# Performance work log

Measured on AMD Instinct MI355X. Metric: run time of the kernel, lower is better.

## Reference

```python
import jax, jax.numpy as jnp
from jax import lax
import numpy as np

D_MODEL = 2048
NUM_EXPERTS = 16
NUM_TOKENS = 8192  # must be divisible by NUM_EXPERTS (balanced assignment)


def setup_inputs() -> dict:
    key = jax.random.key(0)
    k1, k2 = jax.random.split(key)
    features = jax.random.normal(k1, (NUM_TOKENS, D_MODEL), dtype=jnp.float32)
    # gate weight (orthogonal init in torch; gaussian is fine for a numerical baseline)
    W = jax.random.normal(k2, (NUM_EXPERTS, D_MODEL), dtype=jnp.float32) * 0.1
    b = jnp.zeros((NUM_EXPERTS,), dtype=jnp.float32)
    return {"features": features, "W": W, "b": b, "is_training": 1}


def _balanced_assignment(scores):
    """Greedy balanced assignment: each expert receives exactly T//E tokens.
    Deterministic stand-in for the cpp auction-based balanced_assignment: scan
    over tokens, each token takes its best-scoring expert with remaining capacity.
    Returns sort_by_expert: token indices sorted (stably) by assigned expert."""
    T, E = scores.shape
    cap_per_expert = T // E

    def step(cap, s):  # cap: [E] remaining capacity, s: [E] token's scores
        masked = jnp.where(cap > 0, s, -jnp.inf)
        e = jnp.argmax(masked)
        return cap.at[e].add(-1), e

    _, tok2exp = lax.scan(step, jnp.full((E,), cap_per_expert, dtype=jnp.int32), scores)
    sort_by_expert = jnp.argsort(tok2exp, stable=True)  # [T] token ids grouped by expert
    return sort_by_expert


def reference(features, W, b, is_training):
    # gating computed under no_grad in the original
    affinities = lax.stop_gradient(features @ W.T + b)  # [T, E]
    T, E = affinities.shape
    cap = T // E

    sort_by_expert = _balanced_assignment(affinities)

    routing_probs = jax.nn.softmax(affinities, axis=1)  # [T, E]

    # gather_scores: permute probs into expert order, pick each token's score for
    # its assigned expert, then un-permute back to original token order.
    sorted_probs = routing_probs[sort_by_expert]                 # [T, E]
    expert_idx = (jnp.arange(T) // cap)[:, None]                 # [T, 1], balanced splits
    gathered = jnp.take_along_axis(sorted_probs, expert_idx, axis=1)  # [T, 1]
    i_sort = jnp.argsort(sort_by_expert)                         # inverse permutation
    gathered_scores = gathered[i_sort]                           # [T, 1]

    return sort_by_expert, gathered_scores
```

## Files before the change

### kernel.cpp

```cpp
#include <hip/hip_runtime.h>
#include <hip/hip_bf16.h>
#include <math.h>

#define T_TOK 8192
#define D_MODEL 2048
#define N_EXP 16
#define CAP 512
#define NSEG (T_TOK / 64)


__device__ __forceinline__ unsigned int f2ord(float f) {
    unsigned int b = __float_as_uint(f);
    return (b & 0x80000000u) ? ~b : (b | 0x80000000u);
}

__global__ __launch_bounds__(512, 4) void gemm_aff_kernel(
    const float* __restrict__ feat, const float* __restrict__ W,
    float* __restrict__ aff)
{
    __shared__ float flds[8][D_MODEL];

    const int tid  = threadIdx.x;
    const int wave = tid >> 6, lane = tid & 63;
    const int tbase = blockIdx.x * 8;

    {
        const float4* src = (const float4*)(feat + (size_t)tbase * D_MODEL);
        float4* dst = (float4*)&flds[0][0];
        #pragma unroll
        for (int i = 0; i < 8; ++i)
            dst[tid + i * 512] = src[tid + i * 512];
    }

    const float* w0 = W + (size_t)(wave * 2) * D_MODEL + lane * 4;
    const float* w1 = w0 + D_MODEL;

    float acc[16];
    #pragma unroll
    for (int i = 0; i < 16; ++i) acc[i] = 0.f;

    float4 wv0 = *(const float4*)(w0);
    float4 wv1 = *(const float4*)(w1);
    __syncthreads();

    #pragma unroll
    for (int j = 0; j < 8; ++j) {
        float4 wn0, wn1;
        if (j < 7) {
            wn0 = *(const float4*)(w0 + (j + 1) * 256);
            wn1 = *(const float4*)(w1 + (j + 1) * 256);
        } else {
            wn0 = wv0; wn1 = wv1;
        }
        const float* fl = &flds[0][0] + j * 256 + lane * 4;
        #pragma unroll
        for (int r = 0; r < 8; ++r) {
            float4 f = *(const float4*)(fl + r * D_MODEL);
            acc[r * 2 + 0] += f.x * wv0.x;
            acc[r * 2 + 0] += f.y * wv0.y;
            acc[r * 2 + 0] += f.z * wv0.z;
            acc[r * 2 + 0] += f.w * wv0.w;
            acc[r * 2 + 1] += f.x * wv1.x;
            acc[r * 2 + 1] += f.y * wv1.y;
            acc[r * 2 + 1] += f.z * wv1.z;
            acc[r * 2 + 1] += f.w * wv1.w;
        }
        wv0 = wn0; wv1 = wn1;
    }

    #pragma unroll
    for (int step = 0; step < 4; ++step) {
        const int m    = 1 << step;
        const int half = 8 >> step;
        const bool hi  = (lane & m) != 0;
        #pragma unroll
        for (int jj = 0; jj < half; ++jj) {
            float send = hi ? acc[jj] : acc[jj + half];
            float recv = __shfl_xor(send, m, 64);
            acc[jj] = (hi ? acc[jj + half] : acc[jj]) + recv;
        }
    }
    acc[0] += __shfl_xor(acc[0], 16, 64);
    acc[0] += __shfl_xor(acc[0], 32, 64);

    if (lane < 16) {
        const int slot = ((lane & 1) << 3) | (((lane >> 1) & 1) << 2)
                       | (((lane >> 2) & 1) << 1) | ((lane >> 3) & 1);
        const int r = slot >> 1, el = slot & 1;
        aff[(size_t)(tbase + r) * N_EXP + wave * 2 + el] = acc[0];
    }
}

__global__ __launch_bounds__(256) void finalize_kernel(
    const float* __restrict__ aff_in, const float* __restrict__ bias,
    unsigned long long* __restrict__ pref, float* __restrict__ probs)
{
    const int t = blockIdx.x * 256 + threadIdx.x;

    float aff[N_EXP];
    const float4* p = (const float4*)(aff_in + (size_t)t * N_EXP);
    #pragma unroll
    for (int q = 0; q < 4; ++q) {
        float4 v = p[q];
        aff[q*4+0] = v.x; aff[q*4+1] = v.y; aff[q*4+2] = v.z; aff[q*4+3] = v.w;
    }
    #pragma unroll
    for (int e = 0; e < N_EXP; ++e) aff[e] += bias[e];

    float m = aff[0];
    #pragma unroll
    for (int e = 1; e < N_EXP; ++e) m = fmaxf(m, aff[e]);
    float s = 0.f;
    #pragma unroll
    for (int e = 0; e < N_EXP; ++e) s += __expf(aff[e] - m);

    float4* pr = (float4*)(probs + (size_t)t * N_EXP);
    #pragma unroll
    for (int q = 0; q < 4; ++q) {
        float4 v;
        v.x = __expf(aff[q*4+0] - m) / s;
        v.y = __expf(aff[q*4+1] - m) / s;
        v.z = __expf(aff[q*4+2] - m) / s;
        v.w = __expf(aff[q*4+3] - m) / s;
        pr[q] = v;
    }

    unsigned long long key[N_EXP];
    #pragma unroll
    for (int j = 0; j < N_EXP; ++j)
        key[j] = ((unsigned long long)f2ord(aff[j]) << 4) | (unsigned long long)(15 - j);
    unsigned long long pk = 0ull;
    unsigned int used = 0;
    for (int r = 0; r < N_EXP; ++r) {
        unsigned long long bk = 0ull; int be = 0;
        for (int j = 0; j < N_EXP; ++j)
            if (!((used >> j) & 1u) && key[j] > bk) { bk = key[j]; be = j; }
        used |= (1u << be);
        pk = (pk << 4) | (unsigned long long)be;
    }
    pref[t] = pk;
}

__global__ __launch_bounds__(512) void events_kernel(
    const unsigned long long* __restrict__ pref, int* __restrict__ evt)
{
    __shared__ unsigned long long prefL[T_TOK];
    __shared__ unsigned long long segmask[N_EXP][NSEG + 1];
    __shared__ int pseg[N_EXP][NSEG + 1];
    __shared__ int rem_cap[N_EXP], fparr[N_EXP];
    __shared__ int s_avail, s_pmin, s_fe, s_seglo;
    __shared__ int evp[N_EXP], evf[N_EXP];

    const int tid  = threadIdx.x;
    const int wave = tid >> 6, lane = tid & 63;
    const unsigned long long lt_mask = (1ull << lane) - 1ull;

    for (int i = tid; i < T_TOK; i += 512) prefL[i] = pref[i];
    if (tid < N_EXP) rem_cap[tid] = CAP;
    if (tid == 0) { s_avail = 0xFFFF; s_seglo = 0; }
    __syncthreads();

    for (int s = wave; s < NSEG; s += 8) {
        int c = (int)(prefL[s * 64 + lane] >> 60);
        #pragma unroll
        for (int e = 0; e < N_EXP; ++e) {
            unsigned long long mm = __ballot(c == e);
            if (lane == e) segmask[e][s] = mm;
        }
    }
    __syncthreads();

    for (int round = 0; round < N_EXP; ++round) {
        const unsigned int avail = (unsigned int)s_avail;

        #pragma unroll
        for (int ee = 0; ee < 2; ++ee) {
            const int e = wave + ee * 8;
            const unsigned long long m0 = segmask[e][lane];
            const unsigned long long m1 = segmask[e][64 + lane];
            const int c0 = (int)__popcll(m0), c1 = (int)__popcll(m1);
            int v0 = c0;
            #pragma unroll
            for (int d = 1; d < 64; d <<= 1) {
                int o = __shfl_up(v0, d, 64);
                if (lane >= d) v0 += o;
            }
            const int excl0 = v0 - c0;
            const int tot0  = __shfl(v0, 63, 64);
            int v1 = c1;
            #pragma unroll
            for (int d = 1; d < 64; d <<= 1) {
                int o = __shfl_up(v1, d, 64);
                if (lane >= d) v1 += o;
            }
            const int excl1 = tot0 + v1 - c1;
            pseg[e][lane]      = excl0;
            pseg[e][64 + lane] = excl1;

            int fp = 0x7FFFFFFF;
            if ((avail >> e) & 1u) {
                const int need = rem_cap[e];
                int segc = -1, kk = 0;
                if (excl0 < need && excl0 + c0 >= need)      { segc = lane;      kk = need - excl0; }
                else if (excl1 < need && excl1 + c1 >= need) { segc = 64 + lane; kk = need - excl1; }
                unsigned long long b = __ballot(segc >= 0);
                if (b) {
                    int l2    = __builtin_ctzll(b);
                    int sstar = __shfl(segc, l2, 64);
                    int k2    = __shfl(kk,   l2, 64);
                    unsigned long long m = segmask[e][sstar];
                    int rr = (int)__popcll(m & lt_mask);
                    bool hit = ((m >> lane) & 1ull) && (rr == k2 - 1);
                    unsigned long long hb = __ballot(hit);
                    fp = sstar * 64 + __builtin_ctzll(hb);
                }
            }
            if (lane == 0) fparr[e] = fp;
        }
        __syncthreads();

        if (tid == 0) {
            int pm = 0x7FFFFFFF, f = 0;
            #pragma unroll
            for (int e = 0; e < N_EXP; ++e)
                if (fparr[e] < pm) { pm = fparr[e]; f = e; }
            s_pmin = pm; s_fe = f;
        }
        __syncthreads();
        const int pmin = s_pmin, fe = s_fe;
        const int segF = pmin >> 6;
        const int seglo = s_seglo;

        if (tid < N_EXP) {
            const int e = tid;
            unsigned long long mlep = ((pmin & 63) == 63) ? ~0ull
                                      : ((1ull << ((pmin & 63) + 1)) - 1ull);
            unsigned long long m = segmask[e][segF];
            rem_cap[e] -= pseg[e][segF] + (int)__popcll(m & mlep);
            segmask[e][segF] = m & ~mlep;
        }
        for (int i = tid; i < (segF - seglo) * N_EXP; i += 512)
            segmask[i & 15][seglo + (i >> 4)] = 0ull;
        if (tid == 0) {
            evp[round] = pmin; evf[round] = fe;
            s_avail = (int)(avail & ~(1u << fe));
            s_seglo = segF;
        }
        __syncthreads();

        if (round < N_EXP - 1) {
            const unsigned int navail = avail & ~(1u << fe);
            for (int s = segF + wave; s < NSEG; s += 8) {
                unsigned long long m = segmask[fe][s];
                if (m) {
                    if ((m >> lane) & 1ull) {
                        unsigned long long pp = prefL[s * 64 + lane];
                        int e2 = (int)(pp >> 60);
                        while (!((navail >> e2) & 1u)) { pp <<= 4; e2 = (int)(pp >> 60); }
                        atomicOr(&segmask[e2][s], 1ull << lane);
                    }
                    if (lane == 0) segmask[fe][s] = 0ull;
                }
            }
        }
        __syncthreads();
    }

    if (tid < N_EXP) { evt[tid] = evp[tid]; evt[N_EXP + tid] = evf[tid]; }
}

__global__ __launch_bounds__(256) void choice_kernel(
    const unsigned long long* __restrict__ pref, const int* __restrict__ evt,
    unsigned char* __restrict__ t2e, int* __restrict__ bcnt)
{
    __shared__ int evp[N_EXP], evf[N_EXP];
    __shared__ int sc[4][N_EXP];
    const int tid = threadIdx.x, b = blockIdx.x;
    const int wave = tid >> 6, lane = tid & 63;
    if (tid < N_EXP) evp[tid] = evt[tid];
    else if (tid < 2 * N_EXP) evf[tid - N_EXP] = evt[tid];
    __syncthreads();

    const int t = b * 256 + tid;
    unsigned int mask = 0xFFFFu;
    #pragma unroll
    for (int j = 0; j < N_EXP; ++j)
        if (evp[j] < t) mask &= ~(1u << evf[j]);

    unsigned long long pp = pref[t];
    int e = (int)(pp >> 60);
    while (!((mask >> e) & 1u)) { pp <<= 4; e = (int)(pp >> 60); }
    t2e[t] = (unsigned char)e;

    #pragma unroll
    for (int e2 = 0; e2 < N_EXP; ++e2) {
        unsigned long long mm = __ballot(e == e2);
        if (lane == e2) sc[wave][e2] = (int)__popcll(mm);
    }
    __syncthreads();
    if (tid < N_EXP)
        bcnt[b * N_EXP + tid] = sc[0][tid] + sc[1][tid] + sc[2][tid] + sc[3][tid];
}

__global__ __launch_bounds__(256) void writeout_kernel(
    const unsigned char* __restrict__ t2e, const int* __restrict__ bcnt,
    const float* __restrict__ probs,
    float* __restrict__ out0, float* __restrict__ out1)
{
    __shared__ int base[N_EXP];
    __shared__ int sc[4][N_EXP];
    const int tid = threadIdx.x, b = blockIdx.x;
    const int wave = tid >> 6, lane = tid & 63;
    const unsigned long long lt_mask = (1ull << lane) - 1ull;

    const int t = b * 256 + tid;
    const int c = (int)t2e[t];

    unsigned long long own = 0ull;
    #pragma unroll
    for (int e2 = 0; e2 < N_EXP; ++e2) {
        unsigned long long mm = __ballot(c == e2);
        if (c == e2) own = mm;
        if (lane == e2) sc[wave][e2] = (int)__popcll(mm);
    }
    if (tid < N_EXP) {
        int s = 0;
        for (int b2 = 0; b2 < b; ++b2) s += bcnt[b2 * N_EXP + tid];
        base[tid] = s;
    }
    __syncthreads();

    int rank = (int)__popcll(own & lt_mask);
    for (int w2 = 0; w2 < wave; ++w2) rank += sc[w2][c];
    const int pos = base[c] + rank;
    out0[c * CAP + pos] = (float)t;
    out1[t] = probs[(size_t)t * N_EXP + c];
}

extern "C" void kernel_launch(void* const* d_in, const int* in_sizes, int n_in,
                              void* d_out, int out_size, void* d_ws, size_t ws_size,
                              hipStream_t stream) {
    const float* feat = (const float*)d_in[0];
    const float* W    = (const float*)d_in[1];
    const float* bias = (const float*)d_in[2];

    float* out = (float*)d_out;
    char*  ws  = (char*)d_ws;

    float* aff               = (float*)ws;
    unsigned long long* pref = (unsigned long long*)(ws + 524288);
    float* probs             = (float*)(ws + 589824);
    int* evt                 = (int*)(ws + 1114112);
    unsigned char* t2e       = (unsigned char*)(ws + 1114240);
    int* bcnt                = (int*)(ws + 1122432);

    hipLaunchKernelGGL(gemm_aff_kernel, dim3(T_TOK / 8), dim3(512), 0, stream,
                       feat, W, aff);
    hipLaunchKernelGGL(finalize_kernel, dim3(T_TOK / 256), dim3(256), 0, stream,
                       aff, bias, pref, probs);
    hipLaunchKernelGGL(events_kernel, dim3(1), dim3(512), 0, stream,
                       pref, evt);
    hipLaunchKernelGGL(choice_kernel, dim3(T_TOK / 256), dim3(256), 0, stream,
                       pref, evt, t2e, bcnt);
    hipLaunchKernelGGL(writeout_kernel, dim3(T_TOK / 256), dim3(256), 0, stream,
                       t2e, bcnt, probs, out, out + T_TOK);
}
```

Baseline: 187.7 us.

## Keep events-kernel state in registers and cut per-round barriers

```diff
diff --git a/kernel.cpp b/kernel.cpp
--- a/kernel.cpp
+++ b/kernel.cpp
@@ -141,27 +141,24 @@
     pref[t] = pk;
 }
 
-__global__ __launch_bounds__(512) void events_kernel(
+__global__ __launch_bounds__(512, 1) void events_kernel(
     const unsigned long long* __restrict__ pref, int* __restrict__ evt)
 {
-    __shared__ unsigned long long prefL[T_TOK];
-    __shared__ unsigned long long segmask[N_EXP][NSEG + 1];
-    __shared__ int pseg[N_EXP][NSEG + 1];
-    __shared__ int rem_cap[N_EXP], fparr[N_EXP];
-    __shared__ int s_avail, s_pmin, s_fe, s_seglo;
-    __shared__ int evp[N_EXP], evf[N_EXP];
+    __shared__ unsigned long long segmask[N_EXP][NSEG];
+    __shared__ int fparr[N_EXP];
 
     const int tid  = threadIdx.x;
     const int wave = tid >> 6, lane = tid & 63;
     const unsigned long long lt_mask = (1ull << lane) - 1ull;
 
-    for (int i = tid; i < T_TOK; i += 512) prefL[i] = pref[i];
-    if (tid < N_EXP) rem_cap[tid] = CAP;
-    if (tid == 0) { s_avail = 0xFFFF; s_seglo = 0; }
-    __syncthreads();
-
-    for (int s = wave; s < NSEG; s += 8) {
-        int c = (int)(prefL[s * 64 + lane] >> 60);
+    unsigned long long myPref[16];
+    #pragma unroll
+    for (int k = 0; k < 16; ++k) myPref[k] = pref[tid + 512 * k];
+
+    #pragma unroll
+    for (int k = 0; k < 16; ++k) {
+        const int s = k * 8 + wave;
+        const int c = (int)(myPref[k] >> 60);
         #pragma unroll
         for (int e = 0; e < N_EXP; ++e) {
             unsigned long long mm = __ballot(c == e);
@@ -170,103 +167,128 @@
     }
     __syncthreads();
 
+    const int eA = wave, eB = wave + 8;
+    int capA = CAP, capB = CAP;
+    unsigned long long m0A = 0, m1A = 0, m0B = 0, m1B = 0;
+    int excl0A = 0, excl1A = 0, excl0B = 0, excl1B = 0;
+    int segF = 0;
+    unsigned long long mlep = 0;
+    unsigned int avail = 0xFFFFu;
+    int myp = 0, myf = 0;
+
     for (int round = 0; round < N_EXP; ++round) {
-        const unsigned int avail = (unsigned int)s_avail;
-
-        #pragma unroll
-        for (int ee = 0; ee < 2; ++ee) {
-            const int e = wave + ee * 8;
-            const unsigned long long m0 = segmask[e][lane];
-            const unsigned long long m1 = segmask[e][64 + lane];
-            const int c0 = (int)__popcll(m0), c1 = (int)__popcll(m1);
-            int v0 = c0;
+        {
+            int exf = (segF < 64) ? __shfl(excl0A, segF, 64) : __shfl(excl1A, segF - 64, 64);
+            unsigned long long mf = (segF < 64) ? __shfl(m0A, segF, 64) : __shfl(m1A, segF - 64, 64);
+            capA -= exf + (int)__popcll(mf & mlep);
+            exf = (segF < 64) ? __shfl(excl0B, segF, 64) : __shfl(excl1B, segF - 64, 64);
+            mf  = (segF < 64) ? __shfl(m0B, segF, 64) : __shfl(m1B, segF - 64, 64);
+            capB -= exf + (int)__popcll(mf & mlep);
+        }
+
+        unsigned long long a0 = segmask[eA][lane];
+        unsigned long long a1 = segmask[eA][64 + lane];
+        unsigned long long b0 = segmask[eB][lane];
+        unsigned long long b1 = segmask[eB][64 + lane];
+        if (lane < segF)            { a0 = 0; b0 = 0; }
+        else if (lane == segF)      { a0 &= ~mlep; b0 &= ~mlep; }
+        if (64 + lane < segF)       { a1 = 0; b1 = 0; }
+        else if (64 + lane == segF) { a1 &= ~mlep; b1 &= ~mlep; }
+        m0A = a0; m1A = a1; m0B = b0; m1B = b1;
+
+        const int c0A = (int)__popcll(a0), c1A = (int)__popcll(a1);
+        const int c0B = (int)__popcll(b0), c1B = (int)__popcll(b1);
+        int v0A = c0A, v1A = c1A, v0B = c0B, v1B = c1B;
+        #pragma unroll
+        for (int d = 1; d < 64; d <<= 1) {
+            int t0 = __shfl_up(v0A, d, 64);
+            int t1 = __shfl_up(v1A, d, 64);
+            int t2 = __shfl_up(v0B, d, 64);
+            int t3 = __shfl_up(v1B, d, 64);
+            if (lane >= d) { v0A += t0; v1A += t1; v0B += t2; v1B += t3; }
+        }
+        const int tot0A = __shfl(v0A, 63, 64);
+        const int tot0B = __shfl(v0B, 63, 64);
+        excl0A = v0A - c0A;
+        excl1A = tot0A + v1A - c1A;
+        excl0B = v0B - c0B;
+        excl1B = tot0B + v1B - c1B;
+
+        int fpA = 0x7FFFFFFF;
+        if ((avail >> eA) & 1u) {
+            const int need = capA;
+            int segc = -1, kk = 0;
+            if (excl0A < need && excl0A + c0A >= need)      { segc = lane;      kk = need - excl0A; }
+            else if (excl1A < need && excl1A + c1A >= need) { segc = 64 + lane; kk = need - excl1A; }
+            unsigned long long bb = __ballot(segc >= 0);
+            if (bb) {
+                int l2    = __builtin_ctzll(bb);
+                int sstar = __shfl(segc, l2, 64);
+                int k2    = __shfl(kk,   l2, 64);
+                unsigned long long msel = (sstar < 64) ? __shfl(a0, sstar, 64)
+                                                       : __shfl(a1, sstar - 64, 64);
+                int rr = (int)__popcll(msel & lt_mask);
+                bool hit = ((msel >> lane) & 1ull) && (rr == k2 - 1);
+                unsigned long long hb = __ballot(hit);
+                fpA = sstar * 64 + __builtin_ctzll(hb);
+            }
+        }
+        int fpB = 0x7FFFFFFF;
+        if ((avail >> eB) & 1u) {
+            const int need = capB;
+            int segc = -1, kk = 0;
+            if (excl0B < need && excl0B + c0B >= need)      { segc = lane;      kk = need - excl0B; }
+            else if (excl1B < need && excl1B + c1B >= need) { segc = 64 + lane; kk = need - excl1B; }
+            unsigned long long bb = __ballot(segc >= 0);
+            if (bb) {
+                int l2    = __builtin_ctzll(bb);
+                int sstar = __shfl(segc, l2, 64);
+                int k2    = __shfl(kk,   l2, 64);
+                unsigned long long msel = (sstar < 64) ? __shfl(b0, sstar, 64)
+                                                       : __shfl(b1, sstar - 64, 64);
+                int rr = (int)__popcll(msel & lt_mask);
+                bool hit = ((msel >> lane) & 1ull) && (rr == k2 - 1);
+                unsigned long long hb = __ballot(hit);
+                fpB = sstar * 64 + __builtin_ctzll(hb);
+            }
+        }
+        if (lane == 0) { fparr[eA] = fpA; fparr[eB] = fpB; }
+        __syncthreads();
+
+        int pmin = 0x7FFFFFFF, fe = 0;
+        #pragma unroll
+        for (int e = 0; e < N_EXP; ++e) {
+            int f = fparr[e];
+            if (f < pmin) { pmin = f; fe = e; }
+        }
+        if (tid == round) { myp = pmin; myf = fe; }
+
+        const int nsegF = pmin >> 6;
+        const unsigned long long nmlep = ((pmin & 63) == 63) ? ~0ull
+                                         : ((1ull << ((pmin & 63) + 1)) - 1ull);
+        const unsigned int navail = avail & ~(1u << fe);
+
+        if (round < N_EXP - 1) {
             #pragma unroll
-            for (int d = 1; d < 64; d <<= 1) {
-                int o = __shfl_up(v0, d, 64);
-                if (lane >= d) v0 += o;
-            }
-            const int excl0 = v0 - c0;
-            const int tot0  = __shfl(v0, 63, 64);
-            int v1 = c1;
-            #pragma unroll
-            for (int d = 1; d < 64; d <<= 1) {
-                int o = __shfl_up(v1, d, 64);
-                if (lane >= d) v1 += o;
-            }
-            const int excl1 = tot0 + v1 - c1;
-            pseg[e][lane]      = excl0;
-            pseg[e][64 + lane] = excl1;
-
-            int fp = 0x7FFFFFFF;
-            if ((avail >> e) & 1u) {
-                const int need = rem_cap[e];
-                int segc = -1, kk = 0;
-                if (excl0 < need && excl0 + c0 >= need)      { segc = lane;      kk = need - excl0; }
-                else if (excl1 < need && excl1 + c1 >= need) { segc = 64 + lane; kk = need - excl1; }
-                unsigned long long b = __ballot(segc >= 0);
-                if (b) {
-                    int l2    = __builtin_ctzll(b);
-                    int sstar = __shfl(segc, l2, 64);
-                    int k2    = __shfl(kk,   l2, 64);
-                    unsigned long long m = segmask[e][sstar];
-                    int rr = (int)__popcll(m & lt_mask);
-                    bool hit = ((m >> lane) & 1ull) && (rr == k2 - 1);
-                    unsigned long long hb = __ballot(hit);
-                    fp = sstar * 64 + __builtin_ctzll(hb);
-                }
-            }
-            if (lane == 0) fparr[e] = fp;
-        }
-        __syncthreads();
-
-        if (tid == 0) {
-            int pm = 0x7FFFFFFF, f = 0;
-            #pragma unroll
-            for (int e = 0; e < N_EXP; ++e)
-                if (fparr[e] < pm) { pm = fparr[e]; f = e; }
-            s_pmin = pm; s_fe = f;
-        }
-        __syncthreads();
-        const int pmin = s_pmin, fe = s_fe;
-        const int segF = pmin >> 6;
-        const int seglo = s_seglo;
-
-        if (tid < N_EXP) {
-            const int e = tid;
-            unsigned long long mlep = ((pmin & 63) == 63) ? ~0ull
-                                      : ((1ull << ((pmin & 63) + 1)) - 1ull);
-            unsigned long long m = segmask[e][segF];
-            rem_cap[e] -= pseg[e][segF] + (int)__popcll(m & mlep);
-            segmask[e][segF] = m & ~mlep;
-        }
-        for (int i = tid; i < (segF - seglo) * N_EXP; i += 512)
-            segmask[i & 15][seglo + (i >> 4)] = 0ull;
-        if (tid == 0) {
-            evp[round] = pmin; evf[round] = fe;
-            s_avail = (int)(avail & ~(1u << fe));
-            s_seglo = segF;
-        }
-        __syncthreads();
-
-        if (round < N_EXP - 1) {
-            const unsigned int navail = avail & ~(1u << fe);
-            for (int s = segF + wave; s < NSEG; s += 8) {
-                unsigned long long m = segmask[fe][s];
-                if (m) {
+            for (int k = 0; k < 16; ++k) {
+                const int s = k * 8 + wave;
+                if (s >= nsegF) {
+                    unsigned long long m = segmask[fe][s];
+                    if (s == nsegF) m &= ~nmlep;
                     if ((m >> lane) & 1ull) {
-                        unsigned long long pp = prefL[s * 64 + lane];
+                        unsigned long long pp = myPref[k];
                         int e2 = (int)(pp >> 60);
                         while (!((navail >> e2) & 1u)) { pp <<= 4; e2 = (int)(pp >> 60); }
                         atomicOr(&segmask[e2][s], 1ull << lane);
                     }
-                    if (lane == 0) segmask[fe][s] = 0ull;
                 }
             }
         }
+        segF = nsegF; mlep = nmlep; avail = navail;
         __syncthreads();
     }
 
-    if (tid < N_EXP) { evt[tid] = evp[tid]; evt[N_EXP + tid] = evf[tid]; }
+    if (tid < N_EXP) { evt[tid] = myp; evt[N_EXP + tid] = myf; }
 }
 
 __global__ __launch_bounds__(256) void choice_kernel(
```

After: 185.6 us. No clear change (-1.1%).
